# Kernel tuning notes

Measured on AMD Instinct MI355X. Metric: run time of the kernel, lower is better.

The kernel has to match this reference:

```python
import jax, jax.numpy as jnp
import numpy as np

NUM_HEADS = 16
NEG = -1000000.0


def setup_inputs() -> dict:
    key = jax.random.key(0)
    ks = jax.random.split(key, 10)
    B, S, H = 2, 2048, 2048
    inp = {
        "X": jax.random.normal(ks[0], (B, S, H), dtype=jnp.float32),
        "attention_mask": jax.random.randint(ks[1], (B, S), 0, 2, dtype=jnp.int32),
    }
    names = ["W_q", "W_k", "W_v", "W_q_m", "W_k_m", "W_v_m", "W_o"]
    for i, n in enumerate(names):
        # matches torch.randn(H, H) / 100 init scale
        inp[n] = jax.random.normal(ks[2 + i], (H, H), dtype=jnp.float32) / 100.0
    return inp


def reference(X, attention_mask, W_q, W_k, W_v, W_q_m, W_k_m, W_v_m, W_o):
    B, S, H = X.shape
    nh, hd = NUM_HEADS, H // NUM_HEADS

    Q = X @ W_q
    K = X @ W_k
    V = X @ W_v
    Q_m = Q @ W_q_m
    K_m = K @ W_k_m
    V_m = V @ W_v_m

    # Faithful to the original: reshape (B, S, H) -> (B, nh, S, H/nh)
    # (row-major reshape, i.e. a sequence-chunked 'head' split, NOT a
    # standard feature-dim head split).
    Qs = Q_m.reshape(B, nh, S, hd)
    Ks = K_m.reshape(B, nh, S, hd)
    Vs = V_m.reshape(B, nh, S, hd)

    # scores: (B, nh, S, S)
    scores = jnp.einsum("bhqd,bhkd->bhqk", Qs, Ks)

    m1 = attention_mask[:, None, :, None]  # (B,1,S,1)
    m2 = attention_mask[:, None, None, :]  # (B,1,1,S)
    scores = jnp.where(m1 == 0, NEG, scores)
    scores = jnp.where(m2 == 0, NEG, scores)

    weights = jax.nn.softmax(scores, axis=-1)
    out = jnp.einsum("bhqk,bhkd->bhqd", weights, Vs)  # (B, nh, S, hd)
    out = out.reshape(B, S, H)  # faithful inverse reshape
    return out @ W_o
```

## Files before the change

### kernel.cpp

```cpp
#include <hip/hip_runtime.h>
#include <hip/hip_bf16.h>

typedef __bf16 bf16x8 __attribute__((ext_vector_type(8)));
typedef float f32x4 __attribute__((ext_vector_type(4)));
typedef unsigned short u16;

__device__ __forceinline__ u16 f2bf(float f) {
  __bf16 b = (__bf16)f;
  return __builtin_bit_cast(u16, b);
}
__device__ __forceinline__ float bf2f(u16 v) {
  unsigned int u = ((unsigned int)v) << 16;
  return __builtin_bit_cast(float, u);
}

struct PrepArgs {
  const float* X; u16* Xb;
  const float* Wsrc[3]; u16* Wdst[3];
  const float* Tsrc[3]; u16* Tdst[3];
};

__global__ void prep(PrepArgs a) {
  __shared__ float t[32][33];
  const int blk = blockIdx.x, tid = threadIdx.x;
  if (blk < 8192) {
    int i = blk * 256 + tid;
    float4 f = reinterpret_cast<const float4*>(a.X)[i];
    ushort4 o;
    o.x = f2bf(f.x); o.y = f2bf(f.y); o.z = f2bf(f.z); o.w = f2bf(f.w);
    reinterpret_cast<ushort4*>(a.Xb)[i] = o;
  } else if (blk < 20480) {
    int r = blk - 8192;
    int z = r >> 12;
    int i = (r & 4095) * 256 + tid;
    float4 f = reinterpret_cast<const float4*>(a.Wsrc[z])[i];
    ushort4 o;
    o.x = f2bf(f.x); o.y = f2bf(f.y); o.z = f2bf(f.z); o.w = f2bf(f.w);
    reinterpret_cast<ushort4*>(a.Wdst[z])[i] = o;
  } else {
    int r = blk - 20480;
    int z = r >> 12;
    int rem = r & 4095;
    int bx = rem & 63, by = rem >> 6;
    const float* src = a.Tsrc[z];
    u16* dst = a.Tdst[z];
    int tx = tid & 31, ty = tid >> 5;
#pragma unroll
    for (int i = 0; i < 4; ++i)
      t[ty + i * 8][tx] = src[(size_t)(by * 32 + ty + i * 8) * 2048 + bx * 32 + tx];
    __syncthreads();
#pragma unroll
    for (int i = 0; i < 4; ++i)
      dst[(size_t)(bx * 32 + ty + i * 8) * 2048 + by * 32 + tx] = f2bf(t[tx][ty + i * 8]);
  }
}

__global__ void post_transpose(const u16* __restrict__ Vm, u16* __restrict__ VT,
                               const float* __restrict__ Wo, u16* __restrict__ WoT) {
  __shared__ u16 ts[32][33];
  __shared__ float tf[32][33];
  const int blk = blockIdx.x, tid = threadIdx.x;
  const int tx = tid & 31, ty = tid >> 5;
  if (blk < 8192) {
    int slab = blk >> 8;
    int rem = blk & 255;
    int bx = rem & 63, by = rem >> 6;
    const u16* s = Vm + (size_t)slab * 2048 * 128;
    u16* d = VT + (size_t)slab * 128 * 2048;
#pragma unroll
    for (int i = 0; i < 4; ++i)
      ts[ty + i * 8][tx] = s[(size_t)(bx * 32 + ty + i * 8) * 128 + by * 32 + tx];
    __syncthreads();
#pragma unroll
    for (int i = 0; i < 4; ++i)
      d[(size_t)(by * 32 + ty + i * 8) * 2048 + bx * 32 + tx] = ts[tx][ty + i * 8];
  } else {
    int rem = blk - 8192;
    int bx = rem & 63, by = rem >> 6;
#pragma unroll
    for (int i = 0; i < 4; ++i)
      tf[ty + i * 8][tx] = Wo[(size_t)(by * 32 + ty + i * 8) * 2048 + bx * 32 + tx];
    __syncthreads();
#pragma unroll
    for (int i = 0; i < 4; ++i)
      WoT[(size_t)(bx * 32 + ty + i * 8) * 2048 + by * 32 + tx] = f2bf(tf[tx][ty + i * 8]);
  }
}

struct GemmArgs { const u16* A[3]; const u16* B[3]; void* C[3]; };

#define SBARF() do { __builtin_amdgcn_sched_barrier(0); __builtin_amdgcn_s_barrier(); \
                     __builtin_amdgcn_sched_barrier(0); } while (0)
#define LGKM0() do { asm volatile("s_waitcnt lgkmcnt(0)" ::: "memory"); \
                     __builtin_amdgcn_sched_barrier(0); } while (0)
#define VMC4()  do { asm volatile("s_waitcnt vmcnt(4)" ::: "memory"); \
                     __builtin_amdgcn_sched_barrier(0); } while (0)
#define VMC0()  do { asm volatile("s_waitcnt vmcnt(0)" ::: "memory"); \
                     __builtin_amdgcn_sched_barrier(0); } while (0)

__device__ __forceinline__ void gll16(const u16* gp, u16* lp) {
  __builtin_amdgcn_global_load_lds((const __attribute__((address_space(1))) void*)gp,
                                   (__attribute__((address_space(3))) void*)lp, 16, 0, 0);
}

#define MQUAD(A0_, A1_, M0_, M1_) do { \
    __builtin_amdgcn_s_setprio(1); \
    _Pragma("unroll") for (int s_ = 0; s_ < 2; ++s_) \
      _Pragma("unroll") for (int nt = 0; nt < 4; ++nt) { \
        acc[M0_][nt] = __builtin_amdgcn_mfma_f32_16x16x32_bf16(A0_[s_], bF[nt][s_], acc[M0_][nt], 0, 0, 0); \
        acc[M1_][nt] = __builtin_amdgcn_mfma_f32_16x16x32_bf16(A1_[s_], bF[nt][s_], acc[M1_][nt], 0, 0, 0); } \
    __builtin_amdgcn_s_setprio(0); \
    __builtin_amdgcn_sched_barrier(0); \
  } while (0)

template <bool F32OUT>
__global__ __launch_bounds__(512, 2)
void gemm8(GemmArgs g, int M, int N, int K) {
  (void)M;
  extern __shared__ u16 lds[];
  const u16* A = g.A[blockIdx.z];
  const u16* B = g.B[blockIdx.z];
  const int tid = threadIdx.x;
  const int lane = tid & 63, w = tid >> 6;
  const int wm = w >> 2, wn = w & 3;
  const int l15 = lane & 15, quad = lane >> 4;
  const int m0 = blockIdx.y * 256, n0 = blockIdx.x * 256;

  const int srow = tid & 127;
  const int sks8 = (tid >> 7) * 8;
  const int swu = w * 512;

  auto stage = [&](int buf, int mat, int half, int kt) {
    const u16* src = mat ? B : A;
    const size_t g0 = (size_t)((mat ? n0 : m0) + half * 128 + srow) * K
                    + (size_t)kt * 64 + sks8;
    u16* l0 = lds + buf * 32768 + (mat * 2 + half) * 8192 + swu;
    gll16(src + g0, l0);
    gll16(src + g0 + 32, l0 + 4096);
  };

  const int aoff = wm * 8192 + quad * 1024 + l15 * 8;
  const int boff = 16384 + (wn >> 1) * 8192 + quad * 1024 + ((wn & 1) * 64 + l15) * 8;

  const f32x4 zf = {0.f, 0.f, 0.f, 0.f};
  f32x4 acc[8][4];
#pragma unroll
  for (int i = 0; i < 8; ++i)
#pragma unroll
    for (int j = 0; j < 4; ++j) acc[i][j] = zf;

  bf16x8 aP[2][2], aR[6][2], bF[4][2];

#define LDB_ALL8(buf_) do { _Pragma("unroll") for (int nt = 0; nt < 4; ++nt) { \
    const u16* p_ = lds + (buf_) * 32768 + boff + nt * 128; \
    bF[nt][0] = *reinterpret_cast<const bf16x8*>(p_); \
    bF[nt][1] = *reinterpret_cast<const bf16x8*>(p_ + 4096); } } while (0)
#define LDA2_8(buf_) do { _Pragma("unroll") for (int mi = 0; mi < 2; ++mi) { \
    const u16* p_ = lds + (buf_) * 32768 + aoff + mi * 128; \
    aP[mi][0] = *reinterpret_cast<const bf16x8*>(p_); \
    aP[mi][1] = *reinterpret_cast<const bf16x8*>(p_ + 4096); } } while (0)
#define LDA6_8(buf_) do { _Pragma("unroll") for (int mi = 0; mi < 6; ++mi) { \
    const u16* p_ = lds + (buf_) * 32768 + aoff + (mi + 2) * 128; \
    aR[mi][0] = *reinterpret_cast<const bf16x8*>(p_); \
    aR[mi][1] = *reinterpret_cast<const bf16x8*>(p_ + 4096); } } while (0)

  const int NT = K >> 6;
  const int NI = NT >> 1;

  stage(0, 0, 0, 0); stage(0, 0, 1, 0); stage(0, 1, 0, 0); stage(0, 1, 1, 0);
  stage(1, 0, 0, 1); stage(1, 0, 1, 1);
  VMC4();
  SBARF();

  for (int i = 0; i < NI; ++i) {
    const int te = 2 * i, to = te + 1;
    const bool pf = (i + 1 < NI);
    LDB_ALL8(0); LDA2_8(0);
    stage(1, 1, 0, to);
    SBARF(); LGKM0();
    MQUAD(aP[0], aP[1], 0, 1);
    SBARF();
    LDA6_8(0);
    stage(1, 1, 1, to);
    SBARF(); LGKM0();
    MQUAD(aR[0], aR[1], 2, 3);
    SBARF();
    if (pf) stage(0, 0, 0, te + 2);
    SBARF();
    MQUAD(aR[2], aR[3], 4, 5);
    SBARF();
    if (pf) stage(0, 0, 1, te + 2);
    SBARF();
    MQUAD(aR[4], aR[5], 6, 7);
    if (pf) { VMC4(); } else { VMC0(); }
    SBARF();
    LDB_ALL8(1); LDA2_8(1);
    if (pf) stage(0, 1, 0, te + 2);
    SBARF(); LGKM0();
    MQUAD(aP[0], aP[1], 0, 1);
    SBARF();
    LDA6_8(1);
    if (pf) stage(0, 1, 1, te + 2);
    SBARF(); LGKM0();
    MQUAD(aR[0], aR[1], 2, 3);
    SBARF();
    if (pf) stage(1, 0, 0, to + 2);
    SBARF();
    MQUAD(aR[2], aR[3], 4, 5);
    SBARF();
    if (pf) stage(1, 0, 1, to + 2);
    SBARF();
    MQUAD(aR[4], aR[5], 6, 7);
    VMC4();
    SBARF();
  }

#pragma unroll
  for (int mt = 0; mt < 8; ++mt)
#pragma unroll
    for (int nt = 0; nt < 4; ++nt)
#pragma unroll
      for (int r = 0; r < 4; ++r) {
        int mrow = m0 + wm * 128 + mt * 16 + quad * 4 + r;
        int ncol = n0 + wn * 64 + nt * 16 + l15;
        if constexpr (F32OUT)
          ((float*)g.C[blockIdx.z])[(size_t)mrow * N + ncol] = acc[mt][nt][r];
        else
          ((u16*)g.C[blockIdx.z])[(size_t)mrow * N + ncol] = f2bf(acc[mt][nt][r]);
      }
#undef LDB_ALL8
#undef LDA2_8
#undef LDA6_8
}

__global__ __launch_bounds__(512, 2)
void flash_attn(const u16* __restrict__ Qm, const u16* __restrict__ Km,
                const u16* __restrict__ VTr, const int* __restrict__ mask,
                u16* __restrict__ Out) {
  extern __shared__ u16 lds[];
  const int b = blockIdx.z, head = blockIdx.y, qb = blockIdx.x;
  const int slab = b * 16 + head;
  const u16* Qs = Qm + (size_t)slab * 2048 * 128;
  const u16* Kg = Km + (size_t)slab * 2048 * 128;
  const u16* Vg = VTr + (size_t)slab * 128 * 2048;
  u16* Og = Out + (size_t)slab * 2048 * 128;
  const int* mb = mask + b * 2048;

  const int tid = threadIdx.x;
  const int lane = tid & 63, w = tid >> 6;
  const int l15 = lane & 15, quad = lane >> 4;
  const int q0w = qb * 256 + w * 32;

  u16* Mf = lds + 49152;
  u16* PLw = lds + 32768 + w * 2048;

#pragma unroll
  for (int j = 0; j < 4; ++j) {
    int i = j * 512 + tid;
    Mf[i] = mb[i] ? (u16)0x3F80 : (u16)0;
  }

  bf16x8 aQ[2][4];
#pragma unroll
  for (int mt = 0; mt < 2; ++mt)
#pragma unroll
    for (int c = 0; c < 4; ++c)
      aQ[mt][c] = *reinterpret_cast<const bf16x8*>(
          Qs + (size_t)(q0w + mt * 16 + l15) * 128 + c * 32 + quad * 8);

  int mq[2][4];
#pragma unroll
  for (int mt = 0; mt < 2; ++mt)
#pragma unroll
    for (int r = 0; r < 4; ++r) mq[mt][r] = mb[q0w + mt * 16 + quad * 4 + r];

  auto stageKV = [&](int buf, int k0) {
#pragma unroll
    for (int t = 0; t < 4; ++t) {
      int idx = w * 4 + t;
      if (idx < 16) {
        const u16* gp = Kg + (size_t)(k0 + lane) * 128 + idx * 8;
        gll16(gp, lds + buf * 8192 + idx * 512);
      } else {
        int u = idx - 16, kc = u >> 1, dh = u & 1;
        const u16* gp = Vg + (size_t)(dh * 64 + lane) * 2048 + k0 + kc * 8;
        gll16(gp, lds + 16384 + buf * 8192 + (kc * 128 + dh * 64) * 8);
      }
    }
  };

  const f32x4 zf = {0.f, 0.f, 0.f, 0.f};
  float l_part[2][4];
  f32x4 acc[2][8];
#pragma unroll
  for (int mt = 0; mt < 2; ++mt) {
#pragma unroll
    for (int r = 0; r < 4; ++r) l_part[mt][r] = 0.f;
#pragma unroll
    for (int nd = 0; nd < 8; ++nd) acc[mt][nd] = zf;
  }

  stageKV(0, 0);
  __syncthreads();

  for (int t = 0; t < 32; ++t) {
    const int cur = t & 1;
    const int k0 = t * 64;
    if (t + 1 < 32) stageKV(cur ^ 1, k0 + 64);

    const u16* Ks = lds + cur * 8192;
    const u16* Vs = lds + 16384 + cur * 8192;

    f32x4 st[2][4];
#pragma unroll
    for (int mt = 0; mt < 2; ++mt)
#pragma unroll
      for (int nt = 0; nt < 4; ++nt) st[mt][nt] = zf;
#pragma unroll
    for (int c = 0; c < 4; ++c)
#pragma unroll
      for (int nt = 0; nt < 4; ++nt) {
        bf16x8 bK = *reinterpret_cast<const bf16x8*>(
            &Ks[((c * 4 + quad) * 64 + nt * 16 + l15) * 8]);
        st[0][nt] = __builtin_amdgcn_mfma_f32_16x16x32_bf16(aQ[0][c], bK, st[0][nt], 0, 0, 0);
        st[1][nt] = __builtin_amdgcn_mfma_f32_16x16x32_bf16(aQ[1][c], bK, st[1][nt], 0, 0, 0);
      }

    float mkf[4];
#pragma unroll
    for (int nt = 0; nt < 4; ++nt) mkf[nt] = bf2f(Mf[k0 + nt * 16 + l15]);

#pragma unroll
    for (int mt = 0; mt < 2; ++mt)
#pragma unroll
      for (int nt = 0; nt < 4; ++nt)
#pragma unroll
        for (int r = 0; r < 4; ++r) {
          float e = __expf(st[mt][nt][r]) * mkf[nt];
          float p = mq[mt][r] ? e : 1.0f;
          l_part[mt][r] += p;
          int row = mt * 16 + quad * 4 + r;
          int col = nt * 16 + l15;
          int addr = row * 64 + (((col >> 3) ^ (row & 7)) << 3) + (col & 7);
          PLw[addr] = f2bf(p);
        }

#pragma unroll
    for (int pc = 0; pc < 2; ++pc) {
      bf16x8 aP0 = *reinterpret_cast<const bf16x8*>(
          &PLw[(0 + l15) * 64 + (((pc * 4 + quad) ^ (l15 & 7)) << 3)]);
      bf16x8 aP1 = *reinterpret_cast<const bf16x8*>(
          &PLw[(16 + l15) * 64 + (((pc * 4 + quad) ^ (l15 & 7)) << 3)]);
#pragma unroll
      for (int nd = 0; nd < 8; ++nd) {
        bf16x8 bV = *reinterpret_cast<const bf16x8*>(
            &Vs[((pc * 4 + quad) * 128 + nd * 16 + l15) * 8]);
        acc[0][nd] = __builtin_amdgcn_mfma_f32_16x16x32_bf16(aP0, bV, acc[0][nd], 0, 0, 0);
        acc[1][nd] = __builtin_amdgcn_mfma_f32_16x16x32_bf16(aP1, bV, acc[1][nd], 0, 0, 0);
      }
    }

    VMC0();
    SBARF();
  }

  float inv[2][4];
#pragma unroll
  for (int mt = 0; mt < 2; ++mt)
#pragma unroll
    for (int r = 0; r < 4; ++r) {
      float l = l_part[mt][r];
      l += __shfl_xor(l, 1, 16);
      l += __shfl_xor(l, 2, 16);
      l += __shfl_xor(l, 4, 16);
      l += __shfl_xor(l, 8, 16);
      inv[mt][r] = 1.0f / l;
    }
#pragma unroll
  for (int mt = 0; mt < 2; ++mt)
#pragma unroll
    for (int nd = 0; nd < 8; ++nd)
#pragma unroll
      for (int r = 0; r < 4; ++r)
        Og[(size_t)(q0w + mt * 16 + quad * 4 + r) * 128 + nd * 16 + l15] =
            f2bf(acc[mt][nd][r] * inv[mt][r]);
}

extern "C" void kernel_launch(void* const* d_in, const int* in_sizes, int n_in,
                              void* d_out, int out_size, void* d_ws, size_t ws_size,
                              hipStream_t stream) {
  const float* X    = (const float*)d_in[0];
  const int*   mask = (const int*)d_in[1];
  const float* W_q  = (const float*)d_in[2];
  const float* W_k  = (const float*)d_in[3];
  const float* W_v  = (const float*)d_in[4];
  const float* W_qm = (const float*)d_in[5];
  const float* W_km = (const float*)d_in[6];
  const float* W_vm = (const float*)d_in[7];
  const float* W_o  = (const float*)d_in[8];
  float* out = (float*)d_out;

  char* ws = (char*)d_ws;
  const size_t MB = 1ull << 20;
  u16* Xb    = (u16*)(ws);
  u16* Wc0   = (u16*)(ws + 16 * MB);
  u16* Wc1   = (u16*)(ws + 24 * MB);
  u16* Wc2   = (u16*)(ws + 32 * MB);
  u16* WmT0  = (u16*)(ws + 40 * MB);
  u16* WmT1  = (u16*)(ws + 48 * MB);
  u16* WmT2  = (u16*)(ws + 56 * MB);
  u16* WqqT0 = (u16*)(ws + 64 * MB);
  u16* WqqT1 = (u16*)(ws + 72 * MB);
  u16* WqqT2 = (u16*)(ws + 80 * MB);
  u16* Qm    = (u16*)(ws + 88 * MB);
  u16* Km    = (u16*)(ws + 104 * MB);
  u16* Vm    = (u16*)(ws + 120 * MB);
  u16* VT    = Wc0;
  u16* AO    = WmT0;
  u16* WoT   = WqqT0;

  static bool attr_done = false;
  if (!attr_done) {
    (void)hipFuncSetAttribute(reinterpret_cast<const void*>(&gemm8<false>),
                              hipFuncAttributeMaxDynamicSharedMemorySize, 131072);
    (void)hipFuncSetAttribute(reinterpret_cast<const void*>(&gemm8<true>),
                              hipFuncAttributeMaxDynamicSharedMemorySize, 131072);
    (void)hipFuncSetAttribute(reinterpret_cast<const void*>(&flash_attn),
                              hipFuncAttributeMaxDynamicSharedMemorySize, 102400);
    attr_done = true;
  }

  {
    PrepArgs a;
    a.X = X; a.Xb = Xb;
    a.Wsrc[0] = W_q;  a.Wsrc[1] = W_k;  a.Wsrc[2] = W_v;
    a.Wdst[0] = Wc0;  a.Wdst[1] = Wc1;  a.Wdst[2] = Wc2;
    a.Tsrc[0] = W_qm; a.Tsrc[1] = W_km; a.Tsrc[2] = W_vm;
    a.Tdst[0] = WmT0; a.Tdst[1] = WmT1; a.Tdst[2] = WmT2;
    prep<<<dim3(32768), dim3(256), 0, stream>>>(a);
  }

  {
    GemmArgs g{{WmT0, WmT1, WmT2}, {Wc0, Wc1, Wc2}, {WqqT0, WqqT1, WqqT2}};
    gemm8<false><<<dim3(8, 8, 3), dim3(512), 131072, stream>>>(g, 2048, 2048, 2048);
  }

  {
    GemmArgs g{{Xb, Xb, Xb}, {WqqT0, WqqT1, WqqT2}, {Qm, Km, Vm}};
    gemm8<false><<<dim3(8, 16, 3), dim3(512), 131072, stream>>>(g, 4096, 2048, 2048);
  }

  post_transpose<<<dim3(12288), dim3(256), 0, stream>>>(Vm, VT, W_o, WoT);

  flash_attn<<<dim3(8, 16, 2), dim3(512), 102400, stream>>>(Qm, Km, VT, mask, AO);

  {
    GemmArgs g{{AO, AO, AO}, {WoT, WoT, WoT}, {out, out, out}};
    gemm8<true><<<dim3(8, 16, 1), dim3(512), 131072, stream>>>(g, 4096, 2048, 2048);
  }
}
```

Measured before the change: 551.0 us.

## Rebalance GEMM LDS/global-load interleaving and raise MFMA priority in attention

The GEMM main loop now loads A fragments two M-tiles at a time instead of 2 then 6, cutting live registers. It also reorders staging so B halves are fetched first and spreads global-to-LDS copies evenly across the four MFMA quads. An early lgkmcnt(8) wait before the barrier is added. Separately, the flash-attention kernel wraps both MFMA blocks in s_setprio(1) so those waves get priority over the softmax phase of other waves. The risk is more LDS-read round trips and barriers per iteration, and a staging order that depends on the buffer-consumption assumptions being correct.

```diff
diff --git a/kernel.cpp b/kernel.cpp
--- a/kernel.cpp
+++ b/kernel.cpp
@@ -93,6 +93,8 @@
                      __builtin_amdgcn_sched_barrier(0); } while (0)
 #define LGKM0() do { asm volatile("s_waitcnt lgkmcnt(0)" ::: "memory"); \
                      __builtin_amdgcn_sched_barrier(0); } while (0)
+#define LGKM8() do { asm volatile("s_waitcnt lgkmcnt(8)" ::: "memory"); \
+                     __builtin_amdgcn_sched_barrier(0); } while (0)
 #define VMC4()  do { asm volatile("s_waitcnt vmcnt(4)" ::: "memory"); \
                      __builtin_amdgcn_sched_barrier(0); } while (0)
 #define VMC0()  do { asm volatile("s_waitcnt vmcnt(0)" ::: "memory"); \
@@ -149,68 +151,68 @@
 #pragma unroll
     for (int j = 0; j < 4; ++j) acc[i][j] = zf;
 
-  bf16x8 aP[2][2], aR[6][2], bF[4][2];
+  bf16x8 aA[2][2], bF[4][2];
 
 #define LDB_ALL8(buf_) do { _Pragma("unroll") for (int nt = 0; nt < 4; ++nt) { \
     const u16* p_ = lds + (buf_) * 32768 + boff + nt * 128; \
     bF[nt][0] = *reinterpret_cast<const bf16x8*>(p_); \
     bF[nt][1] = *reinterpret_cast<const bf16x8*>(p_ + 4096); } } while (0)
-#define LDA2_8(buf_) do { _Pragma("unroll") for (int mi = 0; mi < 2; ++mi) { \
-    const u16* p_ = lds + (buf_) * 32768 + aoff + mi * 128; \
-    aP[mi][0] = *reinterpret_cast<const bf16x8*>(p_); \
-    aP[mi][1] = *reinterpret_cast<const bf16x8*>(p_ + 4096); } } while (0)
-#define LDA6_8(buf_) do { _Pragma("unroll") for (int mi = 0; mi < 6; ++mi) { \
-    const u16* p_ = lds + (buf_) * 32768 + aoff + (mi + 2) * 128; \
-    aR[mi][0] = *reinterpret_cast<const bf16x8*>(p_); \
-    aR[mi][1] = *reinterpret_cast<const bf16x8*>(p_ + 4096); } } while (0)
+#define LDA_PAIR(buf_, mb_) do { _Pragma("unroll") for (int mi = 0; mi < 2; ++mi) { \
+    const u16* p_ = lds + (buf_) * 32768 + aoff + ((mb_) + mi) * 128; \
+    aA[mi][0] = *reinterpret_cast<const bf16x8*>(p_); \
+    aA[mi][1] = *reinterpret_cast<const bf16x8*>(p_ + 4096); } } while (0)
 
   const int NT = K >> 6;
   const int NI = NT >> 1;
 
-  stage(0, 0, 0, 0); stage(0, 0, 1, 0); stage(0, 1, 0, 0); stage(0, 1, 1, 0);
-  stage(1, 0, 0, 1); stage(1, 0, 1, 1);
+  stage(0, 1, 0, 0); stage(0, 1, 1, 0); stage(0, 0, 0, 0); stage(0, 0, 1, 0);
+  stage(1, 1, 0, 1); stage(1, 1, 1, 1);
   VMC4();
   SBARF();
 
   for (int i = 0; i < NI; ++i) {
     const int te = 2 * i, to = te + 1;
-    const bool pf = (i + 1 < NI);
-    LDB_ALL8(0); LDA2_8(0);
-    stage(1, 1, 0, to);
-    SBARF(); LGKM0();
-    MQUAD(aP[0], aP[1], 0, 1);
-    SBARF();
-    LDA6_8(0);
-    stage(1, 1, 1, to);
-    SBARF(); LGKM0();
-    MQUAD(aR[0], aR[1], 2, 3);
-    SBARF();
+    const bool pf = (te + 2 < NT);
+    LDB_ALL8(0); LDA_PAIR(0, 0);
+    stage(1, 0, 0, to);
+    LGKM8(); SBARF(); LGKM0();
+    MQUAD(aA[0], aA[1], 0, 1);
+    SBARF();
+    LDA_PAIR(0, 2);
+    stage(1, 0, 1, to);
+    SBARF(); LGKM0();
+    MQUAD(aA[0], aA[1], 2, 3);
+    SBARF();
+    LDA_PAIR(0, 4);
+    if (pf) stage(0, 1, 0, te + 2);
+    SBARF(); LGKM0();
+    MQUAD(aA[0], aA[1], 4, 5);
+    SBARF();
+    LDA_PAIR(0, 6);
+    if (pf) stage(0, 1, 1, te + 2);
+    SBARF(); LGKM0();
+    MQUAD(aA[0], aA[1], 6, 7);
+    if (pf) { VMC4(); } else { VMC0(); }
+    SBARF();
+    LDB_ALL8(1); LDA_PAIR(1, 0);
     if (pf) stage(0, 0, 0, te + 2);
-    SBARF();
-    MQUAD(aR[2], aR[3], 4, 5);
-    SBARF();
+    LGKM8(); SBARF(); LGKM0();
+    MQUAD(aA[0], aA[1], 0, 1);
+    SBARF();
+    LDA_PAIR(1, 2);
     if (pf) stage(0, 0, 1, te + 2);
-    SBARF();
-    MQUAD(aR[4], aR[5], 6, 7);
-    if (pf) { VMC4(); } else { VMC0(); }
-    SBARF();
-    LDB_ALL8(1); LDA2_8(1);
-    if (pf) stage(0, 1, 0, te + 2);
-    SBARF(); LGKM0();
-    MQUAD(aP[0], aP[1], 0, 1);
-    SBARF();
-    LDA6_8(1);
-    if (pf) stage(0, 1, 1, te + 2);
-    SBARF(); LGKM0();
-    MQUAD(aR[0], aR[1], 2, 3);
-    SBARF();
-    if (pf) stage(1, 0, 0, to + 2);
-    SBARF();
-    MQUAD(aR[2], aR[3], 4, 5);
-    SBARF();
-    if (pf) stage(1, 0, 1, to + 2);
-    SBARF();
-    MQUAD(aR[4], aR[5], 6, 7);
+    SBARF(); LGKM0();
+    MQUAD(aA[0], aA[1], 2, 3);
+    SBARF();
+    LDA_PAIR(1, 4);
+    if (pf) stage(1, 1, 0, to + 2);
+    SBARF(); LGKM0();
+    MQUAD(aA[0], aA[1], 4, 5);
+    SBARF();
+    LDA_PAIR(1, 6);
+    if (pf) stage(1, 1, 1, to + 2);
+    SBARF(); LGKM0();
+    MQUAD(aA[0], aA[1], 6, 7);
     VMC4();
     SBARF();
   }
@@ -229,8 +231,7 @@
           ((u16*)g.C[blockIdx.z])[(size_t)mrow * N + ncol] = f2bf(acc[mt][nt][r]);
       }
 #undef LDB_ALL8
-#undef LDA2_8
-#undef LDA6_8
+#undef LDA_PAIR
 }
 
 __global__ __launch_bounds__(512, 2)
@@ -316,6 +317,7 @@
     for (int mt = 0; mt < 2; ++mt)
 #pragma unroll
       for (int nt = 0; nt < 4; ++nt) st[mt][nt] = zf;
+    __builtin_amdgcn_s_setprio(1);
 #pragma unroll
     for (int c = 0; c < 4; ++c)
 #pragma unroll
@@ -325,6 +327,7 @@
         st[0][nt] = __builtin_amdgcn_mfma_f32_16x16x32_bf16(aQ[0][c], bK, st[0][nt], 0, 0, 0);
         st[1][nt] = __builtin_amdgcn_mfma_f32_16x16x32_bf16(aQ[1][c], bK, st[1][nt], 0, 0, 0);
       }
+    __builtin_amdgcn_s_setprio(0);
 
     float mkf[4];
 #pragma unroll
@@ -345,6 +348,7 @@
           PLw[addr] = f2bf(p);
         }
 
+    __builtin_amdgcn_s_setprio(1);
 #pragma unroll
     for (int pc = 0; pc < 2; ++pc) {
       bf16x8 aP0 = *reinterpret_cast<const bf16x8*>(
@@ -359,6 +363,7 @@
         acc[1][nd] = __builtin_amdgcn_mfma_f32_16x16x32_bf16(aP1, bV, acc[1][nd], 0, 0, 0);
       }
     }
+    __builtin_amdgcn_s_setprio(0);
 
     VMC0();
     SBARF();
```

Measured after the change: 549.6 us. Within noise of the previous version (-0.2%).
